# Optimization experiments

Measured on AMD Instinct MI355X. Metric: run time of the kernel, lower is better.

Reference implementation:

```python
import jax, jax.numpy as jnp
import numpy as np

N = 50000       # nodes
E = 1600000     # edges (before self-loops)
H = 4           # heads
C = 32          # channels per head
G = 64          # graphs in batch
NEG_SLOPE = 0.2


def gat_conv(x, src, dst, W, att_src, att_dst, bias):
    # x: [N, Fin]; W: [Fin, H*C]; att_*: [H, C]; bias: [H*C]
    h = (x @ W).reshape(N, H, C)                       # [N, H, C]
    a_src = jnp.einsum('nhc,hc->nh', h, att_src)       # [N, H]
    a_dst = jnp.einsum('nhc,hc->nh', h, att_dst)       # [N, H]
    e = a_src[src] + a_dst[dst]                        # [E', H]
    e = jax.nn.leaky_relu(e, NEG_SLOPE)
    # softmax over incoming edges of each destination node
    m = jax.ops.segment_max(e, dst, num_segments=N)    # [N, H]
    ex = jnp.exp(e - m[dst])
    denom = jax.ops.segment_sum(ex, dst, num_segments=N)  # [N, H]
    alpha = ex / (denom[dst] + 1e-16)                  # [E', H]
    msg = h[src] * alpha[:, :, None]                   # [E', H, C]
    out = jax.ops.segment_sum(msg, dst, num_segments=N)  # [N, H, C]
    return out.reshape(N, H * C) + bias


def setup_inputs() -> dict:
    key = jax.random.key(0)
    ks = jax.random.split(key, 12)
    x = jax.random.normal(ks[0], (N, 128), dtype=jnp.float32)
    edge_index = jax.random.randint(ks[1], (2, E), 0, N, dtype=jnp.int64)
    batch = jnp.sort(jax.random.randint(ks[2], (N,), 0, G, dtype=jnp.int64))
    s = 0.05
    return {
        'x': x,
        'edge_index': edge_index,
        'batch': batch,
        'W1': jax.random.normal(ks[3], (128, H * C), dtype=jnp.float32) * s,
        'att_src1': jax.random.normal(ks[4], (H, C), dtype=jnp.float32) * s,
        'att_dst1': jax.random.normal(ks[5], (H, C), dtype=jnp.float32) * s,
        'b1': jnp.zeros((H * C,), dtype=jnp.float32),
        'W2': jax.random.normal(ks[6], (H * C, H * C), dtype=jnp.float32) * s,
        'att_src2': jax.random.normal(ks[7], (H, C), dtype=jnp.float32) * s,
        'att_dst2': jax.random.normal(ks[8], (H, C), dtype=jnp.float32) * s,
        'b2': jnp.zeros((H * C,), dtype=jnp.float32),
        'fc_W': jax.random.normal(ks[9], (H * C, 8), dtype=jnp.float32) * s,
        'fc_b': jnp.zeros((8,), dtype=jnp.float32),
    }


def reference(x, edge_index, batch, W1, att_src1, att_dst1, b1,
              W2, att_src2, att_dst2, b2, fc_W, fc_b):
    # add self loops (PyG GATConv default)
    ar = jnp.arange(N, dtype=edge_index.dtype)
    src = jnp.concatenate([edge_index[0], ar])
    dst = jnp.concatenate([edge_index[1], ar])
    h = gat_conv(x, src, dst, W1, att_src1, att_dst1, b1)
    h = jax.nn.elu(h)
    h = gat_conv(h, src, dst, W2, att_src2, att_dst2, b2)
    # global mean pool over graphs
    sums = jax.ops.segment_sum(h, batch, num_segments=G)          # [G, HC]
    cnt = jax.ops.segment_sum(jnp.ones((N,), h.dtype), batch, num_segments=G)
    pooled = sums / jnp.maximum(cnt, 1.0)[:, None]
    logits = pooled @ fc_W + fc_b                                  # [G, 8]
    return jax.nn.log_softmax(logits, axis=1)
```

## Files before the change

### kernel.cpp

```cpp
#include <hip/hip_runtime.h>
#include <math.h>

#define HC 128
#define GG 64
#define NEG 0.2f
#define TILE 8192
#define BW 128
#define SLOT 8192
#define NBMAX 512
#define LDA 136
#define PPARTS 8

typedef __attribute__((ext_vector_type(8))) short short8;
typedef __attribute__((ext_vector_type(4))) float floatx4;
typedef __attribute__((ext_vector_type(2))) float floatx2;

static __device__ __forceinline__ float leaky(float x) { return x > 0.f ? x : NEG * x; }

static __device__ __forceinline__ unsigned short f2bf(float f) {
    unsigned u = __float_as_uint(f);
    u += 0x7FFF + ((u >> 16) & 1);
    return (unsigned short)(u >> 16);
}
static __device__ __forceinline__ float bf2f(unsigned short s) {
    return __uint_as_float(((unsigned)s) << 16);
}

#if __has_builtin(__builtin_amdgcn_cvt_pk_f32_fp8) && __has_builtin(__builtin_amdgcn_cvt_pk_fp8_f32)
template <bool HI>
static __device__ __forceinline__ floatx2 fp8pair(unsigned int w) {
    return __builtin_amdgcn_cvt_pk_f32_fp8((int)w, HI);
}
static __device__ __forceinline__ unsigned int f32x2_fp8(float a, float b) {
    return ((unsigned int)__builtin_amdgcn_cvt_pk_fp8_f32(a, b, 0, false)) & 0xFFFFu;
}
#else
static __device__ __forceinline__ float fp8one(unsigned v) {
    unsigned e = (v >> 3) & 15u, m = v & 7u;
    float mag = e ? __uint_as_float(((e + 120u) << 23) | (m << 20))
                  : (float)m * 0.001953125f;
    return (v & 0x80u) ? -mag : mag;
}
template <bool HI>
static __device__ __forceinline__ floatx2 fp8pair(unsigned int w) {
    unsigned h = HI ? (w >> 16) : w;
    floatx2 r; r.x = fp8one(h & 0xFFu); r.y = fp8one((h >> 8) & 0xFFu);
    return r;
}
static __device__ __forceinline__ unsigned fp8enc(float f) {
    unsigned u = __float_as_uint(f);
    unsigned s = (u >> 24) & 0x80u;
    float a = fabsf(f);
    if (a >= 448.f) return s | 0x7Eu;
    if (a < 0.015625f) {
        unsigned m = (unsigned)(int)rintf(a * 512.f);
        return s | m;
    }
    u = __float_as_uint(a);
    u += 0xFFFFFu + ((u >> 20) & 1u);
    unsigned e8 = (u >> 23) - 120u;
    if (e8 >= 16u) return s | 0x7Eu;
    return s | (e8 << 3) | ((u >> 20) & 7u);
}
static __device__ __forceinline__ unsigned int f32x2_fp8(float a, float b) {
    return fp8enc(a) | (fp8enc(b) << 8);
}
#endif

__global__ void init_k(int* __restrict__ gbcur, int NB) {
    int i = blockIdx.x * 256 + threadIdx.x;
    if (i < NB) gbcur[i] = i * SLOT;
}

__global__ __launch_bounds__(256) void prep_w(const float* __restrict__ W1,
                                              const float* __restrict__ W2,
                                              unsigned short* __restrict__ Wt1,
                                              unsigned short* __restrict__ Wt2) {
    const float* W = blockIdx.y ? W2 : W1;
    unsigned short* Wt = blockIdx.y ? Wt2 : Wt1;
    int d = blockIdx.x * 256 + threadIdx.x;
    int j = d & 7;
    int m = (d >> 3) & 15;
    int qf = d >> 7;
    int q = qf & 3;
    int f = qf >> 2;
    int kb = f & 3;
    int ct = f >> 2;
    int n = ct * 16 + m;
    int k = kb * 32 + q * 8 + j;
    Wt[d] = f2bf(W[k * 128 + n]);
}

__global__ __launch_bounds__(256) void binscat_k(const int* __restrict__ ei,
                                                 int* __restrict__ gbcur,
                                                 unsigned int* __restrict__ staging,
                                                 int E, int M, int NB) {
    __shared__ unsigned int reorder[TILE];
    __shared__ int s_cnt[NBMAX], s_off[NBMAX], s_run[NBMAX];
    __shared__ int s_wsum[8];
    __shared__ int s_carry;
    const int tid = threadIdx.x;
    const int lane = tid & 63, wid = tid >> 6;
    const int tbase = blockIdx.x * TILE;
    const int tcnt = min(TILE, M - tbase);

    for (int i = tid; i < NB; i += 256) s_cnt[i] = 0;
    if (tid == 0) s_carry = 0;
    __syncthreads();

    for (int t = tid; t < tcnt; t += 256) {
        int i = tbase + t;
        int dst = (i < E) ? ei[E + i] : (i - E);
        atomicAdd(&s_cnt[dst >> 7], 1);
    }
    __syncthreads();

    for (int base = 0; base < NB; base += 256) {
        int i = base + tid;
        int v = (i < NB) ? s_cnt[i] : 0;
        int incl = v;
        #pragma unroll
        for (int off = 1; off < 64; off <<= 1) {
            int u = __shfl_up(incl, off);
            if (lane >= off) incl += u;
        }
        if (lane == 63) s_wsum[wid] = incl;
        __syncthreads();
        if (tid == 0) {
            int a = 0;
            for (int w = 0; w < 4; w++) { int tv = s_wsum[w]; s_wsum[w] = a; a += tv; }
            s_wsum[4] = a;
        }
        __syncthreads();
        int excl = s_carry + s_wsum[wid] + incl - v;
        if (i < NB) s_off[i] = excl;
        __syncthreads();
        if (tid == 0) s_carry += s_wsum[4];
        __syncthreads();
    }

    for (int b = tid; b < NB; b += 256)
        s_run[b] = atomicAdd(&gbcur[b], s_cnt[b]);
    for (int b = tid; b < NB; b += 256) s_cnt[b] = s_off[b];
    __syncthreads();

    for (int t = tid; t < tcnt; t += 256) {
        int i = tbase + t;
        int src, dst;
        if (i < E) { src = ei[i]; dst = ei[E + i]; }
        else       { src = dst = i - E; }
        unsigned int p = ((unsigned int)dst << 16) | (unsigned int)src;
        int r = atomicAdd(&s_cnt[dst >> 7], 1);
        reorder[r] = p;
    }
    __syncthreads();

    for (int t = tid; t < tcnt; t += 256) {
        unsigned int p = reorder[t];
        int b = p >> 23;
        staging[s_run[b] + (t - s_off[b])] = p;
    }
}

__global__ __launch_bounds__(512) void scanb_k(const int* __restrict__ gbcur,
                                               int* __restrict__ bucket_base,
                                               int* __restrict__ row_start,
                                               int NB, int M, int Nn) {
    __shared__ int s_w[8];
    int t = threadIdx.x;
    int v = (t < NB) ? (gbcur[t] - t * SLOT) : 0;
    int incl = v;
    #pragma unroll
    for (int off = 1; off < 64; off <<= 1) {
        int u = __shfl_up(incl, off);
        if ((t & 63) >= off) incl += u;
    }
    if ((t & 63) == 63) s_w[t >> 6] = incl;
    __syncthreads();
    if (t == 0) {
        int a = 0;
        for (int w = 0; w < 8; w++) { int tv = s_w[w]; s_w[w] = a; a += tv; }
        row_start[Nn] = M;
    }
    __syncthreads();
    if (t < NB) bucket_base[t] = s_w[t >> 6] + incl - v;
}

__global__ __launch_bounds__(256) void unbin_k(const unsigned int* __restrict__ staging,
                                               const int* __restrict__ gbcur,
                                               const int* __restrict__ bucket_base,
                                               int* __restrict__ row_start,
                                               unsigned short* __restrict__ srcs, int Nn) {
    __shared__ int s_cnt[BW];
    __shared__ int s_cur[BW];
    __shared__ int s_w[2];
    int b = blockIdx.x, t = threadIdx.x;
    int sbase = b * SLOT;
    int cnt = gbcur[b] - sbase;
    int bb = bucket_base[b];
    int n0 = b * BW;
    if (t < BW) s_cnt[t] = 0;
    __syncthreads();
    for (int j = t; j < cnt; j += 256)
        atomicAdd(&s_cnt[(staging[sbase + j] >> 16) & (BW - 1)], 1);
    __syncthreads();
    int v = (t < BW) ? s_cnt[t] : 0;
    int incl = v;
    #pragma unroll
    for (int off = 1; off < 64; off <<= 1) {
        int u = __shfl_up(incl, off);
        if ((t & 63) >= off) incl += u;
    }
    if (t < BW && (t & 63) == 63) s_w[t >> 6] = incl;
    __syncthreads();
    int excl = incl - v + ((t >= 64 && t < BW) ? s_w[0] : 0);
    if (t < BW) {
        s_cur[t] = bb + excl;
        if (n0 + t < Nn) row_start[n0 + t] = bb + excl;
    }
    __syncthreads();
    for (int j = t; j < cnt; j += 256) {
        unsigned int p = staging[sbase + j];
        int ln = (int)(p >> 16) & (BW - 1);
        int r = atomicAdd(&s_cur[ln], 1);
        srcs[r] = (unsigned short)(p & 0xFFFFu);
    }
}

__global__ __launch_bounds__(128) void gemm_fused(const void* __restrict__ Xv,
                                                  int x_f32,
                                                  const unsigned short* __restrict__ Wt,
                                                  const float* __restrict__ att_s,
                                                  const float* __restrict__ att_d,
                                                  unsigned char* __restrict__ H8,
                                                  float* __restrict__ a_src,
                                                  float* __restrict__ a_dst,
                                                  int n_rows) {
    __shared__ unsigned short As[64 * LDA];
    __shared__ unsigned short Ws[16384];
    const int tid = threadIdx.x;
    const int row0 = blockIdx.x * 64;

    for (int i = tid; i < 2048; i += 128)
        ((uint4*)Ws)[i] = ((const uint4*)Wt)[i];
    if (x_f32) {
        const float* X = (const float*)Xv;
        for (int i = tid; i < 2048; i += 128) {
            int r = i >> 5;
            int c4 = (i & 31) << 2;
            int gr = row0 + r;
            float4 v = (gr < n_rows) ? ((const float4*)&X[(size_t)gr * 128])[i & 31]
                                     : make_float4(0.f, 0.f, 0.f, 0.f);
            ushort4 bv = {f2bf(v.x), f2bf(v.y), f2bf(v.z), f2bf(v.w)};
            *(ushort4*)&As[r * LDA + c4] = bv;
        }
    } else {
        const unsigned short* X = (const unsigned short*)Xv;
        for (int i = tid; i < 1024; i += 128) {
            int r = i >> 4;
            int c8 = (i & 15) << 3;
            int gr = row0 + r;
            uint4 v = (gr < n_rows) ? *(const uint4*)&X[(size_t)gr * 128 + c8]
                                    : make_uint4(0, 0, 0, 0);
            *(uint4*)&As[r * LDA + c8] = v;
        }
    }
    __syncthreads();

    const int lane = tid & 63;
    const int wave = tid >> 6;
    const int m = lane & 15;
    const int quad = lane >> 4;
    const int wr0 = wave * 32;

    floatx4 acc[2][8];
    #pragma unroll
    for (int nt = 0; nt < 2; nt++)
        #pragma unroll
        for (int ct = 0; ct < 8; ct++)
            acc[nt][ct] = (floatx4){0.f, 0.f, 0.f, 0.f};

    #pragma unroll
    for (int kb = 0; kb < 4; kb++) {
        short8 x0 = *(const short8*)&As[(wr0 + m) * LDA + kb * 32 + quad * 8];
        short8 x1 = *(const short8*)&As[(wr0 + 16 + m) * LDA + kb * 32 + quad * 8];
        #pragma unroll
        for (int ct = 0; ct < 8; ct++) {
            short8 wf = *(const short8*)&Ws[(((ct * 4 + kb) * 4) + quad) * 128 + m * 8];
            acc[0][ct] = __builtin_amdgcn_mfma_f32_16x16x32_bf16(wf, x0, acc[0][ct], 0, 0, 0);
            acc[1][ct] = __builtin_amdgcn_mfma_f32_16x16x32_bf16(wf, x1, acc[1][ct], 0, 0, 0);
        }
    }

    const int q4 = quad * 4;
    #pragma unroll
    for (int nt = 0; nt < 2; nt++) {
        int node = row0 + wr0 + nt * 16 + m;
        bool vld = node < n_rows;
        float ps[4] = {0.f, 0.f, 0.f, 0.f};
        float pd[4] = {0.f, 0.f, 0.f, 0.f};
        #pragma unroll
        for (int ct = 0; ct < 8; ct++) {
            floatx4 v = acc[nt][ct];
            int c0 = ct * 16 + q4;
            float4 avs = *(const float4*)&att_s[c0];
            float4 avd = *(const float4*)&att_d[c0];
            int h = ct >> 1;
            ps[h] += v[0] * avs.x + v[1] * avs.y + v[2] * avs.z + v[3] * avs.w;
            pd[h] += v[0] * avd.x + v[1] * avd.y + v[2] * avd.z + v[3] * avd.w;
            if (vld) {
                unsigned pk01 = f32x2_fp8(v[0], v[1]);
                unsigned pk23 = f32x2_fp8(v[2], v[3]);
                *(unsigned*)&H8[(size_t)node * 128 + c0] = pk01 | (pk23 << 16);
            }
        }
        #pragma unroll
        for (int h = 0; h < 4; h++) {
            ps[h] += __shfl_xor(ps[h], 16); ps[h] += __shfl_xor(ps[h], 32);
            pd[h] += __shfl_xor(pd[h], 16); pd[h] += __shfl_xor(pd[h], 32);
        }
        if (lane < 16 && vld) {
            float4 s4 = {ps[0], ps[1], ps[2], ps[3]};
            float4 d4 = {pd[0], pd[1], pd[2], pd[3]};
            *(float4*)&a_src[node * 4] = s4;
            *(float4*)&a_dst[node * 4] = d4;
        }
    }
}

__global__ __launch_bounds__(256) void gat_agg(const unsigned char* __restrict__ H8,
                                               const float* __restrict__ a_src,
                                               const float* __restrict__ a_dst,
                                               const int* __restrict__ row_start,
                                               const unsigned short* __restrict__ srcs,
                                               const float* __restrict__ bias,
                                               unsigned short* __restrict__ OUT,
                                               int n_rows, int elu) {
    int n = (blockIdx.x * 256 + threadIdx.x) >> 3;
    if (n >= n_rows) return;
    int li = threadIdx.x & 7;
    int hd = li >> 1;
    int base = row_start[n];
    int end = row_start[n + 1];
    float adh = a_dst[n * 4 + hd];

    floatx2 acc[8];
    #pragma unroll
    for (int k = 0; k < 8; k++) acc[k] = (floatx2){0.f, 0.f};
    float wsum = 0.f;

    int j = base;
    for (; j + 2 <= end; j += 2) {
        int s0 = srcs[j];
        int s1 = srcs[j + 1];
        float e0 = leaky(a_src[s0 * 4 + hd] + adh);
        float e1 = leaky(a_src[s1 * 4 + hd] + adh);
        uint4 d0 = *(const uint4*)&H8[(size_t)s0 * 128 + li * 16];
        uint4 d1 = *(const uint4*)&H8[(size_t)s1 * 128 + li * 16];
        float w0 = __expf(e0);
        float w1 = __expf(e1);
        floatx2 w20 = {w0, w0}, w21 = {w1, w1};
        acc[0] += w20 * fp8pair<false>(d0.x);
        acc[1] += w20 * fp8pair<true>(d0.x);
        acc[2] += w20 * fp8pair<false>(d0.y);
        acc[3] += w20 * fp8pair<true>(d0.y);
        acc[4] += w20 * fp8pair<false>(d0.z);
        acc[5] += w20 * fp8pair<true>(d0.z);
        acc[6] += w20 * fp8pair<false>(d0.w);
        acc[7] += w20 * fp8pair<true>(d0.w);
        acc[0] += w21 * fp8pair<false>(d1.x);
        acc[1] += w21 * fp8pair<true>(d1.x);
        acc[2] += w21 * fp8pair<false>(d1.y);
        acc[3] += w21 * fp8pair<true>(d1.y);
        acc[4] += w21 * fp8pair<false>(d1.z);
        acc[5] += w21 * fp8pair<true>(d1.z);
        acc[6] += w21 * fp8pair<false>(d1.w);
        acc[7] += w21 * fp8pair<true>(d1.w);
        wsum += w0 + w1;
    }
    if (j < end) {
        int s0 = srcs[j];
        float e0 = leaky(a_src[s0 * 4 + hd] + adh);
        float w0 = __expf(e0);
        uint4 d0 = *(const uint4*)&H8[(size_t)s0 * 128 + li * 16];
        floatx2 w20 = {w0, w0};
        acc[0] += w20 * fp8pair<false>(d0.x);
        acc[1] += w20 * fp8pair<true>(d0.x);
        acc[2] += w20 * fp8pair<false>(d0.y);
        acc[3] += w20 * fp8pair<true>(d0.y);
        acc[4] += w20 * fp8pair<false>(d0.z);
        acc[5] += w20 * fp8pair<true>(d0.z);
        acc[6] += w20 * fp8pair<false>(d0.w);
        acc[7] += w20 * fp8pair<true>(d0.w);
        wsum += w0;
    }

    float ih = 1.0f / (wsum + 1e-16f);
    float o[16];
    #pragma unroll
    for (int k = 0; k < 8; k++) {
        float2 bv = *(const float2*)&bias[li * 16 + 2 * k];
        o[2 * k]     = acc[k].x * ih + bv.x;
        o[2 * k + 1] = acc[k].y * ih + bv.y;
    }
    if (elu) {
        #pragma unroll
        for (int k = 0; k < 16; k++) o[k] = o[k] > 0.f ? o[k] : __expf(o[k]) - 1.f;
    }
    unsigned int pk[8];
    #pragma unroll
    for (int k = 0; k < 8; k++)
        pk[k] = ((unsigned)f2bf(o[2 * k + 1]) << 16) | (unsigned)f2bf(o[2 * k]);
    uint4 s0v = {pk[0], pk[1], pk[2], pk[3]};
    uint4 s1v = {pk[4], pk[5], pk[6], pk[7]};
    unsigned short* op = &OUT[(size_t)n * 128 + li * 16];
    *(uint4*)op = s0v;
    *(uint4*)(op + 8) = s1v;
}

__global__ void bounds_k(const int* __restrict__ batch, int* __restrict__ node_end, int n) {
    int i = blockIdx.x * 256 + threadIdx.x;
    if (i >= n) return;
    int b = batch[i];
    if (i == 0) {
        for (int g = 0; g < b; g++) node_end[g] = 0;
    }
    int bn = (i + 1 < n) ? batch[i + 1] : GG;
    for (int g = b; g < bn; g++) node_end[g] = i + 1;
}

__global__ __launch_bounds__(256) void pool_k(const unsigned* __restrict__ H2u,
                                              const int* __restrict__ node_end,
                                              float* __restrict__ partial) {
    __shared__ float ls[4][128];
    int g = blockIdx.x >> 3;
    int p = blockIdx.x & (PPARTS - 1);
    int s = (g > 0) ? node_end[g - 1] : 0;
    int e = node_end[g];
    int cnt = e - s;
    int chunk = (cnt + PPARTS - 1) >> 3;
    int n0 = s + p * chunk;
    int n1 = min(n0 + chunk, e);
    int col = threadIdx.x & 63;
    int nr = threadIdx.x >> 6;
    float ax = 0.f, ay = 0.f;
    for (int n = n0 + nr; n < n1; n += 4) {
        unsigned u = H2u[(size_t)n * 64 + col];
        ax += bf2f((unsigned short)(u & 0xFFFFu));
        ay += bf2f((unsigned short)(u >> 16));
    }
    ls[nr][col * 2] = ax;
    ls[nr][col * 2 + 1] = ay;
    __syncthreads();
    if (threadIdx.x < 128) {
        float v = ls[0][threadIdx.x] + ls[1][threadIdx.x] +
                  ls[2][threadIdx.x] + ls[3][threadIdx.x];
        partial[(size_t)(p * GG + g) * 128 + threadIdx.x] = v;
    }
}

__global__ __launch_bounds__(64) void head_k(const float* __restrict__ partial,
                                             const int* __restrict__ node_end,
                                             const float* __restrict__ fcW,
                                             const float* __restrict__ fcb,
                                             float* __restrict__ out) {
    __shared__ float p[128];
    __shared__ float lg[8];
    int g = blockIdx.x, t = threadIdx.x;
    int c = node_end[g] - (g > 0 ? node_end[g - 1] : 0);
    float cnt = fmaxf((float)c, 1.0f);
    float v0 = 0.f, v1 = 0.f;
    #pragma unroll
    for (int q = 0; q < PPARTS; q++) {
        v0 += partial[(size_t)(q * GG + g) * 128 + t];
        v1 += partial[(size_t)(q * GG + g) * 128 + 64 + t];
    }
    p[t] = v0 / cnt;
    p[t + 64] = v1 / cnt;
    __syncthreads();
    if (t < 8) {
        float s = fcb[t];
        for (int k = 0; k < 128; k++) s += p[k] * fcW[k * 8 + t];
        lg[t] = s;
    }
    __syncthreads();
    if (t == 0) {
        float m = lg[0];
        for (int j = 1; j < 8; j++) m = fmaxf(m, lg[j]);
        float se = 0.f;
        for (int j = 0; j < 8; j++) se += expf(lg[j] - m);
        float lse = logf(se) + m;
        for (int j = 0; j < 8; j++) out[g * 8 + j] = lg[j] - lse;
    }
}

extern "C" void kernel_launch(void* const* d_in, const int* in_sizes, int n_in,
                              void* d_out, int out_size, void* d_ws, size_t ws_size,
                              hipStream_t stream) {
    const float* x    = (const float*)d_in[0];
    const int*   ei   = (const int*)d_in[1];
    const int*   batch= (const int*)d_in[2];
    const float* W1   = (const float*)d_in[3];
    const float* as1  = (const float*)d_in[4];
    const float* ad1  = (const float*)d_in[5];
    const float* b1   = (const float*)d_in[6];
    const float* W2   = (const float*)d_in[7];
    const float* as2  = (const float*)d_in[8];
    const float* ad2  = (const float*)d_in[9];
    const float* b2   = (const float*)d_in[10];
    const float* fcW  = (const float*)d_in[11];
    const float* fcb  = (const float*)d_in[12];
    float* out = (float*)d_out;

    const int Nn = in_sizes[0] / HC;
    const int E  = in_sizes[1] / 2;
    const int M  = E + Nn;
    const int NB = (Nn + BW - 1) / BW;

    char* ws = (char*)d_ws;
    size_t off = 0;
    auto alloc = [&](size_t bytes) -> char* {
        char* p = ws + off;
        off = (off + bytes + 255) & ~(size_t)255;
        return p;
    };
    size_t hB_bytes  = (size_t)Nn * HC * 2;
    size_t stg_bytes = (size_t)NB * SLOT * 4;
    char* hB_region = alloc(hB_bytes > stg_bytes ? hB_bytes : stg_bytes);
    unsigned short* hB      = (unsigned short*)hB_region;
    unsigned int*   staging = (unsigned int*)hB_region;
    unsigned char*  H8      = (unsigned char*)alloc((size_t)Nn * HC);
    float* asrc      = (float*)alloc((size_t)Nn * 4 * 4);
    float* adst      = (float*)alloc((size_t)Nn * 4 * 4);
    unsigned short* srcs = (unsigned short*)alloc((size_t)M * 2);
    int*   row_start = (int*)alloc((size_t)(Nn + 1) * 4);
    float* partial   = (float*)alloc((size_t)PPARTS * GG * HC * 4);
    int*   node_end  = (int*)alloc((size_t)GG * 4);
    int*   gbcur     = (int*)alloc((size_t)NB * 4);
    int*   bbase     = (int*)alloc((size_t)NB * 4);
    unsigned short* Wt1 = (unsigned short*)alloc(16384 * 2);
    unsigned short* Wt2 = (unsigned short*)alloc(16384 * 2);

    init_k<<<(NB + 255) / 256, 256, 0, stream>>>(gbcur, NB);
    prep_w<<<dim3(64, 2), 256, 0, stream>>>(W1, W2, Wt1, Wt2);
    bounds_k<<<(Nn + 255) / 256, 256, 0, stream>>>(batch, node_end, Nn);
    binscat_k<<<(M + TILE - 1) / TILE, 256, 0, stream>>>(ei, gbcur, staging, E, M, NB);
    scanb_k<<<1, 512, 0, stream>>>(gbcur, bbase, row_start, NB, M, Nn);
    unbin_k<<<NB, 256, 0, stream>>>(staging, gbcur, bbase, row_start, srcs, Nn);
    gemm_fused<<<(Nn + 63) / 64, 128, 0, stream>>>(x, 1, Wt1, as1, ad1, H8, asrc, adst, Nn);
    gat_agg<<<(Nn + 31) / 32, 256, 0, stream>>>(H8, asrc, adst, row_start, srcs, b1, hB, Nn, 1);
    gemm_fused<<<(Nn + 63) / 64, 128, 0, stream>>>(hB, 0, Wt2, as2, ad2, H8, asrc, adst, Nn);
    gat_agg<<<(Nn + 31) / 32, 256, 0, stream>>>(H8, asrc, adst, row_start, srcs, b2, hB, Nn, 0);
    pool_k<<<GG * PPARTS, 256, 0, stream>>>((const unsigned*)hB, node_end, partial);
    head_k<<<GG, 64, 0, stream>>>(partial, node_end, fcW, fcb, out);
}
```

Measured before the change: 272.1 us.

## Split fp8 features into head-pair planes and fuse setup kernels

The fp8 feature matrix is now stored as two planes of 64 bytes per node, each holding two heads. Each GAT aggregation runs as two launches, one per plane, so each pass gathers from a smaller working set that fits cache better for the random source reads. The edge softmax work (a_src lookups, exp) is now done twice per edge. Separately, the init, weight-prep and graph-bounds kernels are merged into one setup kernel, and the bucket-base scan is folded into unbin_k, where each block sums the earlier bucket counts itself. This removes kernel launches at the cost of redundant prefix sums.

```diff
diff --git a/kernel.cpp b/kernel.cpp
--- a/kernel.cpp
+++ b/kernel.cpp
@@ -67,28 +67,41 @@
 }
 #endif
 
-__global__ void init_k(int* __restrict__ gbcur, int NB) {
+__global__ __launch_bounds__(256) void setup_k(const float* __restrict__ W1,
+                                               const float* __restrict__ W2,
+                                               unsigned short* __restrict__ Wt1,
+                                               unsigned short* __restrict__ Wt2,
+                                               int* __restrict__ gbcur,
+                                               const int* __restrict__ batch,
+                                               int* __restrict__ node_end,
+                                               int* __restrict__ row_start,
+                                               int NB, int Nn, int M) {
     int i = blockIdx.x * 256 + threadIdx.x;
     if (i < NB) gbcur[i] = i * SLOT;
-}
-
-__global__ __launch_bounds__(256) void prep_w(const float* __restrict__ W1,
-                                              const float* __restrict__ W2,
-                                              unsigned short* __restrict__ Wt1,
-                                              unsigned short* __restrict__ Wt2) {
-    const float* W = blockIdx.y ? W2 : W1;
-    unsigned short* Wt = blockIdx.y ? Wt2 : Wt1;
-    int d = blockIdx.x * 256 + threadIdx.x;
-    int j = d & 7;
-    int m = (d >> 3) & 15;
-    int qf = d >> 7;
-    int q = qf & 3;
-    int f = qf >> 2;
-    int kb = f & 3;
-    int ct = f >> 2;
-    int n = ct * 16 + m;
-    int k = kb * 32 + q * 8 + j;
-    Wt[d] = f2bf(W[k * 128 + n]);
+    if (i == 0) row_start[Nn] = M;
+    if (i < 32768) {
+        const float* W = (i >> 14) ? W2 : W1;
+        unsigned short* Wt = (i >> 14) ? Wt2 : Wt1;
+        int d = i & 16383;
+        int j = d & 7;
+        int m = (d >> 3) & 15;
+        int qf = d >> 7;
+        int q = qf & 3;
+        int f = qf >> 2;
+        int kb = f & 3;
+        int ct = f >> 2;
+        int n = ct * 16 + m;
+        int k = kb * 32 + q * 8 + j;
+        Wt[d] = f2bf(W[k * 128 + n]);
+    }
+    if (i < Nn) {
+        int b = batch[i];
+        if (i == 0) {
+            for (int g = 0; g < b; g++) node_end[g] = 0;
+        }
+        int bn = (i + 1 < Nn) ? batch[i + 1] : GG;
+        for (int g = b; g < bn; g++) node_end[g] = i + 1;
+    }
 }
 
 __global__ __launch_bounds__(256) void binscat_k(const int* __restrict__ ei,
@@ -162,42 +175,26 @@
     }
 }
 
-__global__ __launch_bounds__(512) void scanb_k(const int* __restrict__ gbcur,
-                                               int* __restrict__ bucket_base,
-                                               int* __restrict__ row_start,
-                                               int NB, int M, int Nn) {
-    __shared__ int s_w[8];
-    int t = threadIdx.x;
-    int v = (t < NB) ? (gbcur[t] - t * SLOT) : 0;
-    int incl = v;
-    #pragma unroll
-    for (int off = 1; off < 64; off <<= 1) {
-        int u = __shfl_up(incl, off);
-        if ((t & 63) >= off) incl += u;
-    }
-    if ((t & 63) == 63) s_w[t >> 6] = incl;
-    __syncthreads();
-    if (t == 0) {
-        int a = 0;
-        for (int w = 0; w < 8; w++) { int tv = s_w[w]; s_w[w] = a; a += tv; }
-        row_start[Nn] = M;
-    }
-    __syncthreads();
-    if (t < NB) bucket_base[t] = s_w[t >> 6] + incl - v;
-}
-
 __global__ __launch_bounds__(256) void unbin_k(const unsigned int* __restrict__ staging,
                                                const int* __restrict__ gbcur,
-                                               const int* __restrict__ bucket_base,
                                                int* __restrict__ row_start,
                                                unsigned short* __restrict__ srcs, int Nn) {
     __shared__ int s_cnt[BW];
     __shared__ int s_cur[BW];
-    __shared__ int s_w[2];
+    __shared__ int s_w[4];
     int b = blockIdx.x, t = threadIdx.x;
     int sbase = b * SLOT;
     int cnt = gbcur[b] - sbase;
-    int bb = bucket_base[b];
+
+    int pacc = 0;
+    for (int i = t; i < b; i += 256) pacc += gbcur[i] - i * SLOT;
+    #pragma unroll
+    for (int off = 1; off < 64; off <<= 1) pacc += __shfl_xor(pacc, off);
+    if ((t & 63) == 0) s_w[t >> 6] = pacc;
+    __syncthreads();
+    int bb = s_w[0] + s_w[1] + s_w[2] + s_w[3];
+    __syncthreads();
+
     int n0 = b * BW;
     if (t < BW) s_cnt[t] = 0;
     __syncthreads();
@@ -240,6 +237,7 @@
     __shared__ unsigned short Ws[16384];
     const int tid = threadIdx.x;
     const int row0 = blockIdx.x * 64;
+    const size_t pstride = (size_t)n_rows * 64;
 
     for (int i = tid; i < 2048; i += 128)
         ((uint4*)Ws)[i] = ((const uint4*)Wt)[i];
@@ -311,7 +309,8 @@
             if (vld) {
                 unsigned pk01 = f32x2_fp8(v[0], v[1]);
                 unsigned pk23 = f32x2_fp8(v[2], v[3]);
-                *(unsigned*)&H8[(size_t)node * 128 + c0] = pk01 | (pk23 << 16);
+                *(unsigned*)&H8[(size_t)(ct >> 2) * pstride + (size_t)node * 64 + (c0 & 63)]
+                    = pk01 | (pk23 << 16);
             }
         }
         #pragma unroll
@@ -328,18 +327,18 @@
     }
 }
 
-__global__ __launch_bounds__(256) void gat_agg(const unsigned char* __restrict__ H8,
+__global__ __launch_bounds__(256) void gat_agg(const unsigned char* __restrict__ H8p,
                                                const float* __restrict__ a_src,
                                                const float* __restrict__ a_dst,
                                                const int* __restrict__ row_start,
                                                const unsigned short* __restrict__ srcs,
                                                const float* __restrict__ bias,
                                                unsigned short* __restrict__ OUT,
-                                               int n_rows, int elu) {
-    int n = (blockIdx.x * 256 + threadIdx.x) >> 3;
+                                               int n_rows, int elu, int plane) {
+    int n = (blockIdx.x * 256 + threadIdx.x) >> 2;
     if (n >= n_rows) return;
-    int li = threadIdx.x & 7;
-    int hd = li >> 1;
+    int li = threadIdx.x & 3;
+    int hd = plane * 2 + (li >> 1);
     int base = row_start[n];
     int end = row_start[n + 1];
     float adh = a_dst[n * 4 + hd];
@@ -355,8 +354,8 @@
         int s1 = srcs[j + 1];
         float e0 = leaky(a_src[s0 * 4 + hd] + adh);
         float e1 = leaky(a_src[s1 * 4 + hd] + adh);
-        uint4 d0 = *(const uint4*)&H8[(size_t)s0 * 128 + li * 16];
-        uint4 d1 = *(const uint4*)&H8[(size_t)s1 * 128 + li * 16];
+        uint4 d0 = *(const uint4*)&H8p[(size_t)s0 * 64 + li * 16];
+        uint4 d1 = *(const uint4*)&H8p[(size_t)s1 * 64 + li * 16];
         float w0 = __expf(e0);
         float w1 = __expf(e1);
         floatx2 w20 = {w0, w0}, w21 = {w1, w1};
@@ -382,7 +381,7 @@
         int s0 = srcs[j];
         float e0 = leaky(a_src[s0 * 4 + hd] + adh);
         float w0 = __expf(e0);
-        uint4 d0 = *(const uint4*)&H8[(size_t)s0 * 128 + li * 16];
+        uint4 d0 = *(const uint4*)&H8p[(size_t)s0 * 64 + li * 16];
         floatx2 w20 = {w0, w0};
         acc[0] += w20 * fp8pair<false>(d0.x);
         acc[1] += w20 * fp8pair<true>(d0.x);
@@ -399,7 +398,7 @@
     float o[16];
     #pragma unroll
     for (int k = 0; k < 8; k++) {
-        float2 bv = *(const float2*)&bias[li * 16 + 2 * k];
+        float2 bv = *(const float2*)&bias[plane * 64 + li * 16 + 2 * k];
         o[2 * k]     = acc[k].x * ih + bv.x;
         o[2 * k + 1] = acc[k].y * ih + bv.y;
     }
@@ -413,20 +412,9 @@
         pk[k] = ((unsigned)f2bf(o[2 * k + 1]) << 16) | (unsigned)f2bf(o[2 * k]);
     uint4 s0v = {pk[0], pk[1], pk[2], pk[3]};
     uint4 s1v = {pk[4], pk[5], pk[6], pk[7]};
-    unsigned short* op = &OUT[(size_t)n * 128 + li * 16];
+    unsigned short* op = &OUT[(size_t)n * 128 + plane * 64 + li * 16];
     *(uint4*)op = s0v;
     *(uint4*)(op + 8) = s1v;
-}
-
-__global__ void bounds_k(const int* __restrict__ batch, int* __restrict__ node_end, int n) {
-    int i = blockIdx.x * 256 + threadIdx.x;
-    if (i >= n) return;
-    int b = batch[i];
-    if (i == 0) {
-        for (int g = 0; g < b; g++) node_end[g] = 0;
-    }
-    int bn = (i + 1 < n) ? batch[i + 1] : GG;
-    for (int g = b; g < bn; g++) node_end[g] = i + 1;
 }
 
 __global__ __launch_bounds__(256) void pool_k(const unsigned* __restrict__ H2u,
@@ -537,20 +525,22 @@
     float* partial   = (float*)alloc((size_t)PPARTS * GG * HC * 4);
     int*   node_end  = (int*)alloc((size_t)GG * 4);
     int*   gbcur     = (int*)alloc((size_t)NB * 4);
-    int*   bbase     = (int*)alloc((size_t)NB * 4);
     unsigned short* Wt1 = (unsigned short*)alloc(16384 * 2);
     unsigned short* Wt2 = (unsigned short*)alloc(16384 * 2);
 
-    init_k<<<(NB + 255) / 256, 256, 0, stream>>>(gbcur, NB);
-    prep_w<<<dim3(64, 2), 256, 0, stream>>>(W1, W2, Wt1, Wt2);
-    bounds_k<<<(Nn + 255) / 256, 256, 0, stream>>>(batch, node_end, Nn);
+    const size_t pstr = (size_t)Nn * 64;
+    const int aggrid = (Nn * 4 + 255) / 256;
+
+    setup_k<<<(Nn + 255) / 256, 256, 0, stream>>>(W1, W2, Wt1, Wt2, gbcur, batch,
+                                                  node_end, row_start, NB, Nn, M);
     binscat_k<<<(M + TILE - 1) / TILE, 256, 0, stream>>>(ei, gbcur, staging, E, M, NB);
-    scanb_k<<<1, 512, 0, stream>>>(gbcur, bbase, row_start, NB, M, Nn);
-    unbin_k<<<NB, 256, 0, stream>>>(staging, gbcur, bbase, row_start, srcs, Nn);
+    unbin_k<<<NB, 256, 0, stream>>>(staging, gbcur, row_start, srcs, Nn);
     gemm_fused<<<(Nn + 63) / 64, 128, 0, stream>>>(x, 1, Wt1, as1, ad1, H8, asrc, adst, Nn);
-    gat_agg<<<(Nn + 31) / 32, 256, 0, stream>>>(H8, asrc, adst, row_start, srcs, b1, hB, Nn, 1);
+    gat_agg<<<aggrid, 256, 0, stream>>>(H8,        asrc, adst, row_start, srcs, b1, hB, Nn, 1, 0);
+    gat_agg<<<aggrid, 256, 0, stream>>>(H8 + pstr, asrc, adst, row_start, srcs, b1, hB, Nn, 1, 1);
     gemm_fused<<<(Nn + 63) / 64, 128, 0, stream>>>(hB, 0, Wt2, as2, ad2, H8, asrc, adst, Nn);
-    gat_agg<<<(Nn + 31) / 32, 256, 0, stream>>>(H8, asrc, adst, row_start, srcs, b2, hB, Nn, 0);
+    gat_agg<<<aggrid, 256, 0, stream>>>(H8,        asrc, adst, row_start, srcs, b2, hB, Nn, 0, 0);
+    gat_agg<<<aggrid, 256, 0, stream>>>(H8 + pstr, asrc, adst, row_start, srcs, b2, hB, Nn, 0, 1);
     pool_k<<<GG * PPARTS, 256, 0, stream>>>((const unsigned*)hB, node_end, partial);
     head_k<<<GG, 64, 0, stream>>>(partial, node_end, fcW, fcb, out);
 }
```

After: 318.0 us. 1.17x slower.
